# Performance work log

Hardware: AMD Instinct MI355X
Metric: run time of the kernel (lower is better)

## Reference

```python
import jax, jax.numpy as jnp
from jax import lax
import numpy as np

IN_C, OUT_C = 64, 64
KH = KW = 3
B, H, W = 2, 112, 112


def setup_inputs() -> dict:
    key = jax.random.key(0)
    k1, k2, k3 = jax.random.split(key, 3)
    x = jax.random.normal(k1, (B, IN_C, H, W), dtype=jnp.float32)
    weight = jax.random.normal(k2, (OUT_C, IN_C, KH, KW), dtype=jnp.float32) * 0.05
    bias = jax.random.normal(k3, (OUT_C,), dtype=jnp.float32)
    return {"x": x, "weight": weight, "bias": bias}


def reference(x, weight, bias):
    out_c, in_c, kh, kw = weight.shape
    # preadd grouped conv: channel i*out_c + j uses kernel weight[j, i] on input channel i
    # (matches gen_inout_permutation: perm[i*out_c + j] = i + j*in_c)
    w_grouped = jnp.transpose(weight, (1, 0, 2, 3)).reshape(in_c * out_c, 1, kh, kw)
    preadd = lax.conv_general_dilated(
        x, w_grouped,
        window_strides=(1, 1),
        padding=((1, 1), (1, 1)),
        feature_group_count=in_c,
        dimension_numbers=("NCHW", "OIHW", "NCHW"),
    )  # [B, in_c*out_c, H, W]
    b, _, h, w = preadd.shape
    # permute_add_featuremaps: output channel o = sum_i preadd[:, i*out_c + o]
    added = preadd.reshape(b, in_c, out_c, h, w).sum(axis=1)  # segment reduce over in_c
    return added + bias[None, :, None, None]
```

## Files before the change

kernel.cpp:

```cpp
#include <hip/hip_runtime.h>


#define IN_C  64
#define OUT_C 64
#define BN    2
#define HH    112
#define WW    112
#define HP    114
#define WP    114
#define HW    (HH * WW)
#define NXBLK (BN * HP * 4)
#define NWBLK 36
#define NCONV 392

typedef __attribute__((ext_vector_type(8))) short          bf16x8;
typedef __attribute__((ext_vector_type(8))) unsigned short u16x8;
typedef __attribute__((ext_vector_type(4))) float          f32x4;

static __device__ __forceinline__ unsigned short f2bf(float f) {
    unsigned int u = __builtin_bit_cast(unsigned int, f);
    u += 0x7FFFu + ((u >> 16) & 1u);
    return (unsigned short)(u >> 16);
}

__global__ __launch_bounds__(256) void prep_all(const float* __restrict__ x,
                                                const float* __restrict__ w,
                                                unsigned short* __restrict__ xt,
                                                unsigned short* __restrict__ wt) {
    int blk = blockIdx.x;
    int tid = threadIdx.x;
    if (blk < NXBLK) {
        int cq = blk & 3;
        int r  = blk >> 2;
        int b  = r / HP;
        int yp = r % HP;
        int xp = tid & 127;
        int ch = cq * 16 + (tid >> 7) * 8;
        if (xp >= WP) return;
        unsigned short* dst = xt + (((size_t)b * HP + yp) * WP + xp) * IN_C + ch;
        bool border = (yp == 0) | (yp == HP - 1) | (xp == 0) | (xp == WP - 1);
        if (border) {
            u16x8 z = {0, 0, 0, 0, 0, 0, 0, 0};
            *reinterpret_cast<u16x8*>(dst) = z;
        } else {
            const float* src = x + ((size_t)b * IN_C + ch) * HW + (yp - 1) * WW + (xp - 1);
            u16x8 v;
#pragma unroll
            for (int j = 0; j < 8; ++j)
                v[j] = f2bf(src[(size_t)j * HW]);
            *reinterpret_cast<u16x8*>(dst) = v;
        }
    } else {
        int t = (blk - NXBLK) * 256 + tid;
        f32x4 v = reinterpret_cast<const f32x4*>(w)[t];
#pragma unroll
        for (int j = 0; j < 4; ++j) {
            int e   = 4 * t + j;
            int tap = e % 9;
            int p   = e / 9;
            wt[(size_t)tap * (OUT_C * IN_C) + p] = f2bf(v[j]);
        }
    }
}

__global__ __launch_bounds__(256, 2) void conv_lds(const unsigned short* __restrict__ xt,
                                                   const unsigned short* __restrict__ wt,
                                                   const float* __restrict__ bias,
                                                   float* __restrict__ out) {
    __shared__ unsigned short lw[9 * OUT_C * IN_C];
    int tid = threadIdx.x;
    int blk = blockIdx.x;

#pragma unroll
    for (int i = 0; i < 18; ++i) {
        int V   = tid + i * 256;
        int row = V >> 3;
        int c   = (V & 7) << 3;
        u16x8 v = *reinterpret_cast<const u16x8*>(wt + (size_t)V * 8);
        int cs  = c ^ ((row & 7) << 3);
        *reinterpret_cast<u16x8*>(&lw[row * 64 + cs]) = v;
    }
    __syncthreads();

    int l  = tid & 63;
    int wv = tid >> 6;
    int b  = blk / 196;
    int rm = blk % 196;
    int ytile = rm / 7, xtile = rm % 7;
    int y  = ytile * 4 + wv;
    int x0 = xtile * 16;
    int lm = l & 15;
    int lk = l >> 4;
    int swz = (lm & 7) << 3;

    f32x4 acc0 = {0.f, 0.f, 0.f, 0.f};
    f32x4 acc1 = {0.f, 0.f, 0.f, 0.f};
    f32x4 acc2 = {0.f, 0.f, 0.f, 0.f};
    f32x4 acc3 = {0.f, 0.f, 0.f, 0.f};

    const unsigned short* xb = xt + (((size_t)b * HP + y) * WP + x0 + lm) * IN_C + lk * 8;

#pragma unroll
    for (int r = 0; r < 3; ++r) {
#pragma unroll
        for (int s = 0; s < 3; ++s) {
            const unsigned short* xp  = xb + (r * WP + s) * IN_C;
            int tapbase = ((r * 3 + s) * OUT_C + lm) * 64;
#pragma unroll
            for (int icc = 0; icc < 2; ++icc) {
                int cs = (icc * 32 + lk * 8) ^ swz;
                bf16x8 a  = *reinterpret_cast<const bf16x8*>(xp + icc * 32);
                bf16x8 b0 = *reinterpret_cast<const bf16x8*>(&lw[tapbase + cs]);
                bf16x8 b1 = *reinterpret_cast<const bf16x8*>(&lw[tapbase + 16 * 64 + cs]);
                bf16x8 b2 = *reinterpret_cast<const bf16x8*>(&lw[tapbase + 32 * 64 + cs]);
                bf16x8 b3 = *reinterpret_cast<const bf16x8*>(&lw[tapbase + 48 * 64 + cs]);
                acc0 = __builtin_amdgcn_mfma_f32_16x16x32_bf16(a, b0, acc0, 0, 0, 0);
                acc1 = __builtin_amdgcn_mfma_f32_16x16x32_bf16(a, b1, acc1, 0, 0, 0);
                acc2 = __builtin_amdgcn_mfma_f32_16x16x32_bf16(a, b2, acc2, 0, 0, 0);
                acc3 = __builtin_amdgcn_mfma_f32_16x16x32_bf16(a, b3, acc3, 0, 0, 0);
            }
        }
    }

    f32x4 accs[4] = {acc0, acc1, acc2, acc3};
    int px = x0 + lk * 4;
#pragma unroll
    for (int f = 0; f < 4; ++f) {
        int oc   = f * 16 + lm;
        float bv = bias[oc];
        f32x4 v  = accs[f];
        v.x += bv; v.y += bv; v.z += bv; v.w += bv;
        *reinterpret_cast<f32x4*>(out + (((size_t)b * OUT_C + oc) * HH + y) * WW + px) = v;
    }
}

extern "C" void kernel_launch(void* const* d_in, const int* in_sizes, int n_in,
                              void* d_out, int out_size, void* d_ws, size_t ws_size,
                              hipStream_t stream) {
    const float* x    = (const float*)d_in[0];
    const float* w    = (const float*)d_in[1];
    const float* bias = (const float*)d_in[2];
    float* out        = (float*)d_out;

    unsigned short* xt = (unsigned short*)d_ws;
    unsigned short* wt = xt + (size_t)BN * HP * WP * IN_C;

    prep_all<<<dim3(NXBLK + NWBLK), dim3(256), 0, stream>>>(x, w, xt, wt);
    conv_lds<<<dim3(NCONV), dim3(256), 0, stream>>>(xt, wt, bias, out);
}
```

Before: 18.65 us.

## Switch conv MFMA tiles from 16x16x32 to 32x32x16 with 2x2 wave split

Each wave now computes a 32-pixel by 32-output-channel tile with a single 32x32x16 bf16 MFMA accumulator, instead of a 16-pixel by 64-channel tile built from four 16x16x32 MFMAs. The four waves split the 4x16 block as two output-channel groups times two row pairs. The goal is fewer LDS weight reads and fewer MFMA issues per unit of work. In exchange, the input activations are loaded twice per block (once for each channel-group wave) and the inner loop now runs four K-steps per tap.

```diff
diff --git a/kernel.cpp b/kernel.cpp
--- a/kernel.cpp
+++ b/kernel.cpp
@@ -13,9 +13,10 @@
 #define NWBLK 36
 #define NCONV 392
 
-typedef __attribute__((ext_vector_type(8))) short          bf16x8;
-typedef __attribute__((ext_vector_type(8))) unsigned short u16x8;
-typedef __attribute__((ext_vector_type(4))) float          f32x4;
+typedef __attribute__((ext_vector_type(8)))  short          bf16x8;
+typedef __attribute__((ext_vector_type(8)))  unsigned short u16x8;
+typedef __attribute__((ext_vector_type(4)))  float          f32x4;
+typedef __attribute__((ext_vector_type(16))) float          f32x16;
 
 static __device__ __forceinline__ unsigned short f2bf(float f) {
     unsigned int u = __builtin_bit_cast(unsigned int, f);
@@ -82,55 +83,50 @@
     }
     __syncthreads();
 
-    int l  = tid & 63;
-    int wv = tid >> 6;
-    int b  = blk / 196;
-    int rm = blk % 196;
+    int l   = tid & 63;
+    int wv  = tid >> 6;
+    int ocg = wv & 1;
+    int pxg = wv >> 1;
+    int b   = blk / 196;
+    int rm  = blk % 196;
     int ytile = rm / 7, xtile = rm % 7;
-    int y  = ytile * 4 + wv;
-    int x0 = xtile * 16;
-    int lm = l & 15;
-    int lk = l >> 4;
-    int swz = (lm & 7) << 3;
+    int y0  = ytile * 4 + pxg * 2;
+    int x0  = xtile * 16;
+    int lo  = l & 31;
+    int hi  = l >> 5;
 
-    f32x4 acc0 = {0.f, 0.f, 0.f, 0.f};
-    f32x4 acc1 = {0.f, 0.f, 0.f, 0.f};
-    f32x4 acc2 = {0.f, 0.f, 0.f, 0.f};
-    f32x4 acc3 = {0.f, 0.f, 0.f, 0.f};
+    f32x16 acc = {};
 
-    const unsigned short* xb = xt + (((size_t)b * HP + y) * WP + x0 + lm) * IN_C + lk * 8;
+    const unsigned short* xb =
+        xt + (((size_t)b * HP + y0 + (lo >> 4)) * WP + x0 + (lo & 15)) * IN_C + hi * 8;
+    int ocrow = ocg * 32 + lo;
+    int swzb  = (ocrow & 7) << 3;
 
 #pragma unroll
     for (int r = 0; r < 3; ++r) {
 #pragma unroll
         for (int s = 0; s < 3; ++s) {
-            const unsigned short* xp  = xb + (r * WP + s) * IN_C;
-            int tapbase = ((r * 3 + s) * OUT_C + lm) * 64;
+            const unsigned short* xp = xb + (r * WP + s) * IN_C;
+            int rowbase = ((r * 3 + s) * OUT_C + ocrow) * 64;
 #pragma unroll
-            for (int icc = 0; icc < 2; ++icc) {
-                int cs = (icc * 32 + lk * 8) ^ swz;
-                bf16x8 a  = *reinterpret_cast<const bf16x8*>(xp + icc * 32);
-                bf16x8 b0 = *reinterpret_cast<const bf16x8*>(&lw[tapbase + cs]);
-                bf16x8 b1 = *reinterpret_cast<const bf16x8*>(&lw[tapbase + 16 * 64 + cs]);
-                bf16x8 b2 = *reinterpret_cast<const bf16x8*>(&lw[tapbase + 32 * 64 + cs]);
-                bf16x8 b3 = *reinterpret_cast<const bf16x8*>(&lw[tapbase + 48 * 64 + cs]);
-                acc0 = __builtin_amdgcn_mfma_f32_16x16x32_bf16(a, b0, acc0, 0, 0, 0);
-                acc1 = __builtin_amdgcn_mfma_f32_16x16x32_bf16(a, b1, acc1, 0, 0, 0);
-                acc2 = __builtin_amdgcn_mfma_f32_16x16x32_bf16(a, b2, acc2, 0, 0, 0);
-                acc3 = __builtin_amdgcn_mfma_f32_16x16x32_bf16(a, b3, acc3, 0, 0, 0);
+            for (int ks = 0; ks < 4; ++ks) {
+                bf16x8 a  = *reinterpret_cast<const bf16x8*>(xp + ks * 16);
+                int   cs  = (ks * 16 + hi * 8) ^ swzb;
+                bf16x8 bb = *reinterpret_cast<const bf16x8*>(&lw[rowbase + cs]);
+                acc = __builtin_amdgcn_mfma_f32_32x32x16_bf16(a, bb, acc, 0, 0, 0);
             }
         }
     }
 
-    f32x4 accs[4] = {acc0, acc1, acc2, acc3};
-    int px = x0 + lk * 4;
+    float bv = bias[ocrow];
 #pragma unroll
-    for (int f = 0; f < 4; ++f) {
-        int oc   = f * 16 + lm;
-        float bv = bias[oc];
-        f32x4 v  = accs[f];
-        v.x += bv; v.y += bv; v.z += bv; v.w += bv;
-        *reinterpret_cast<f32x4*>(out + (((size_t)b * OUT_C + oc) * HH + y) * WW + px) = v;
+    for (int g = 0; g < 4; ++g) {
+        int yrow = y0 + (g >> 1);
+        int xcol = x0 + (g & 1) * 8 + hi * 4;
+        f32x4 v;
+#pragma unroll
+        for (int q = 0; q < 4; ++q) v[q] = acc[g * 4 + q] + bv;
+        *reinterpret_cast<f32x4*>(out + (((size_t)b * OUT_C + ocrow) * HH + yrow) * WW + xcol) = v;
     }
 }
 
```

After: 22.54 us. 20.9% more time.

## Split output channels across blocks and give each wave a 2x2 register tile

Applied to the files above, without the earlier changes.

The conv kernel now splits the 64 output channels into two groups of 32, launching twice as many 128-thread blocks. Each wave computes two output rows times two 16-channel tiles, so every input fragment and weight fragment loaded feeds two MFMAs. Block IDs are also remapped so that consecutive launch slots spread across spatial tiles. Each block stages only half the weights in LDS, which cuts LDS usage and allows more blocks per CU and more blocks overall. The cost is that the weights are loaded into LDS by twice as many blocks, and the input rows are read by both channel-group blocks.

```diff
diff --git a/kernel.cpp b/kernel.cpp
--- a/kernel.cpp
+++ b/kernel.cpp
@@ -11,7 +11,7 @@
 #define HW    (HH * WW)
 #define NXBLK (BN * HP * 4)
 #define NWBLK 36
-#define NCONV 392
+#define NCONV 784
 
 typedef __attribute__((ext_vector_type(8))) short          bf16x8;
 typedef __attribute__((ext_vector_type(8))) unsigned short u16x8;
@@ -63,74 +63,92 @@
     }
 }
 
-__global__ __launch_bounds__(256, 2) void conv_lds(const unsigned short* __restrict__ xt,
-                                                   const unsigned short* __restrict__ wt,
-                                                   const float* __restrict__ bias,
-                                                   float* __restrict__ out) {
-    __shared__ unsigned short lw[9 * OUT_C * IN_C];
+__global__ __launch_bounds__(128) void conv_lds(const unsigned short* __restrict__ xt,
+                                                const unsigned short* __restrict__ wt,
+                                                const float* __restrict__ bias,
+                                                float* __restrict__ out) {
+    __shared__ unsigned short lw[9 * 32 * IN_C];
     int tid = threadIdx.x;
-    int blk = blockIdx.x;
+
+    int bid  = blockIdx.x;
+    int wgid = (bid & 7) * 98 + (bid >> 3);
+    int ocg  = wgid & 1;
+    int sp   = wgid >> 1;
+    int b    = sp / 196;
+    int t2   = sp % 196;
+    int ytile = t2 / 7, xtile = t2 % 7;
 
 #pragma unroll
     for (int i = 0; i < 18; ++i) {
-        int V   = tid + i * 256;
-        int row = V >> 3;
-        int c   = (V & 7) << 3;
-        u16x8 v = *reinterpret_cast<const u16x8*>(wt + (size_t)V * 8);
-        int cs  = c ^ ((row & 7) << 3);
-        *reinterpret_cast<u16x8*>(&lw[row * 64 + cs]) = v;
+        int V    = tid + i * 128;
+        int lrow = V >> 3;
+        int c    = (V & 7) << 3;
+        int tap  = lrow >> 5;
+        int ocl  = lrow & 31;
+        u16x8 v  = *reinterpret_cast<const u16x8*>(
+                       wt + ((size_t)(tap << 6) + ocg * 32 + ocl) * IN_C + c);
+        int cs   = c ^ ((ocl & 7) << 3);
+        *reinterpret_cast<u16x8*>(&lw[lrow * IN_C + cs]) = v;
     }
     __syncthreads();
 
     int l  = tid & 63;
     int wv = tid >> 6;
-    int b  = blk / 196;
-    int rm = blk % 196;
-    int ytile = rm / 7, xtile = rm % 7;
-    int y  = ytile * 4 + wv;
+    int y0 = ytile * 4 + wv * 2;
     int x0 = xtile * 16;
     int lm = l & 15;
     int lk = l >> 4;
     int swz = (lm & 7) << 3;
 
-    f32x4 acc0 = {0.f, 0.f, 0.f, 0.f};
-    f32x4 acc1 = {0.f, 0.f, 0.f, 0.f};
-    f32x4 acc2 = {0.f, 0.f, 0.f, 0.f};
-    f32x4 acc3 = {0.f, 0.f, 0.f, 0.f};
+    f32x4 acc00 = {}, acc01 = {}, acc10 = {}, acc11 = {};
 
-    const unsigned short* xb = xt + (((size_t)b * HP + y) * WP + x0 + lm) * IN_C + lk * 8;
+    const unsigned short* xb0 = xt + (((size_t)b * HP + y0)     * WP + x0 + lm) * IN_C + lk * 8;
+    const unsigned short* xb1 = xt + (((size_t)b * HP + y0 + 1) * WP + x0 + lm) * IN_C + lk * 8;
+    int oc0 = ocg * 32 + lm;
+    float bv0 = bias[oc0];
+    float bv1 = bias[oc0 + 16];
 
 #pragma unroll
     for (int r = 0; r < 3; ++r) {
 #pragma unroll
         for (int s = 0; s < 3; ++s) {
-            const unsigned short* xp  = xb + (r * WP + s) * IN_C;
-            int tapbase = ((r * 3 + s) * OUT_C + lm) * 64;
+            const unsigned short* xp0 = xb0 + (r * WP + s) * IN_C;
+            const unsigned short* xp1 = xb1 + (r * WP + s) * IN_C;
+            int rb0 = ((r * 3 + s) * 32 + lm) * IN_C;
 #pragma unroll
             for (int icc = 0; icc < 2; ++icc) {
                 int cs = (icc * 32 + lk * 8) ^ swz;
-                bf16x8 a  = *reinterpret_cast<const bf16x8*>(xp + icc * 32);
-                bf16x8 b0 = *reinterpret_cast<const bf16x8*>(&lw[tapbase + cs]);
-                bf16x8 b1 = *reinterpret_cast<const bf16x8*>(&lw[tapbase + 16 * 64 + cs]);
-                bf16x8 b2 = *reinterpret_cast<const bf16x8*>(&lw[tapbase + 32 * 64 + cs]);
-                bf16x8 b3 = *reinterpret_cast<const bf16x8*>(&lw[tapbase + 48 * 64 + cs]);
-                acc0 = __builtin_amdgcn_mfma_f32_16x16x32_bf16(a, b0, acc0, 0, 0, 0);
-                acc1 = __builtin_amdgcn_mfma_f32_16x16x32_bf16(a, b1, acc1, 0, 0, 0);
-                acc2 = __builtin_amdgcn_mfma_f32_16x16x32_bf16(a, b2, acc2, 0, 0, 0);
-                acc3 = __builtin_amdgcn_mfma_f32_16x16x32_bf16(a, b3, acc3, 0, 0, 0);
+                bf16x8 a0 = *reinterpret_cast<const bf16x8*>(xp0 + icc * 32);
+                bf16x8 a1 = *reinterpret_cast<const bf16x8*>(xp1 + icc * 32);
+                bf16x8 w0 = *reinterpret_cast<const bf16x8*>(&lw[rb0 + cs]);
+                bf16x8 w1 = *reinterpret_cast<const bf16x8*>(&lw[rb0 + 16 * IN_C + cs]);
+                acc00 = __builtin_amdgcn_mfma_f32_16x16x32_bf16(a0, w0, acc00, 0, 0, 0);
+                acc01 = __builtin_amdgcn_mfma_f32_16x16x32_bf16(a0, w1, acc01, 0, 0, 0);
+                acc10 = __builtin_amdgcn_mfma_f32_16x16x32_bf16(a1, w0, acc10, 0, 0, 0);
+                acc11 = __builtin_amdgcn_mfma_f32_16x16x32_bf16(a1, w1, acc11, 0, 0, 0);
             }
         }
     }
 
-    f32x4 accs[4] = {acc0, acc1, acc2, acc3};
     int px = x0 + lk * 4;
+    {
+        f32x4 v;
+        float* o00 = out + (((size_t)b * OUT_C + oc0)      * HH + y0) * WW + px;
+        float* o01 = out + (((size_t)b * OUT_C + oc0 + 16) * HH + y0) * WW + px;
+        float* o10 = o00 + WW;
+        float* o11 = o01 + WW;
 #pragma unroll
-    for (int f = 0; f < 4; ++f) {
-        int oc   = f * 16 + lm;
-        float bv = bias[oc];
-        f32x4 v  = accs[f];
-        v.x += bv; v.y += bv; v.z += bv; v.w += bv;
-        *reinterpret_cast<f32x4*>(out + (((size_t)b * OUT_C + oc) * HH + y) * WW + px) = v;
+        for (int q = 0; q < 4; ++q) v[q] = acc00[q] + bv0;
+        *reinterpret_cast<f32x4*>(o00) = v;
+#pragma unroll
+        for (int q = 0; q < 4; ++q) v[q] = acc01[q] + bv1;
+        *reinterpret_cast<f32x4*>(o01) = v;
+#pragma unroll
+        for (int q = 0; q < 4; ++q) v[q] = acc10[q] + bv0;
+        *reinterpret_cast<f32x4*>(o10) = v;
+#pragma unroll
+        for (int q = 0; q < 4; ++q) v[q] = acc11[q] + bv1;
+        *reinterpret_cast<f32x4*>(o11) = v;
     }
 }
 
@@ -146,5 +164,5 @@
     unsigned short* wt = xt + (size_t)BN * HP * WP * IN_C;
 
     prep_all<<<dim3(NXBLK + NWBLK), dim3(256), 0, stream>>>(x, w, xt, wt);
-    conv_lds<<<dim3(NCONV), dim3(256), 0, stream>>>(xt, wt, bias, out);
+    conv_lds<<<dim3(NCONV), dim3(128), 0, stream>>>(xt, wt, bias, out);
 }
```

New measurement: 19.28 us. 1.03x slower.
